# Performance work log

Hardware: AMD Instinct MI355X
Metric: run time of the kernel (lower is better)

Reference implementation:

```python
import jax, jax.numpy as jnp
import numpy as np

N, E, DIN, DH, H, B = 50000, 800000, 128, 32, 8, 512
NEG_SLOPE = 0.2


def glorot(key, shape):
    fan_in, fan_out = shape[0], shape[-1]
    lim = (6.0 / (fan_in + fan_out)) ** 0.5
    return jax.random.uniform(key, shape, jnp.float32, -lim, lim)


def setup_inputs() -> dict:
    key = jax.random.key(0)
    ks = jax.random.split(key, 16)
    x = jax.random.normal(ks[0], (N, DIN), jnp.float32)
    edge_index = jax.random.randint(ks[1], (2, E), 0, N, jnp.int64)
    batch = jnp.sort(jax.random.randint(ks[2], (N,), 0, B, jnp.int64))
    edge_weight = jax.random.uniform(ks[3], (E, 1), jnp.float32)
    # layer 1: GATv2Conv(DIN -> DH, heads=H, edge_dim=1)
    Wl1 = glorot(ks[4], (DIN, H * DH))
    Wr1 = glorot(ks[5], (DIN, H * DH))
    We1 = glorot(ks[6], (1, H * DH))
    att1 = glorot(ks[7], (H, DH))
    b1 = jnp.zeros((H * DH,), jnp.float32)
    # layer 2: GATv2Conv(H*DH -> DH, heads=1, edge_dim=1)
    Wl2 = glorot(ks[8], (H * DH, DH))
    Wr2 = glorot(ks[9], (H * DH, DH))
    We2 = glorot(ks[10], (1, DH))
    att2 = glorot(ks[11], (1, DH))
    b2 = jnp.zeros((DH,), jnp.float32)
    Wfc = glorot(ks[12], (DH, 1))
    bfc = jnp.zeros((1,), jnp.float32)
    return dict(x=x, edge_index=edge_index, batch=batch, edge_weight=edge_weight,
                Wl1=Wl1, Wr1=Wr1, We1=We1, att1=att1, b1=b1,
                Wl2=Wl2, Wr2=Wr2, We2=We2, att2=att2, b2=b2,
                Wfc=Wfc, bfc=bfc)


def gatv2_layer(x, src, dst, ew, Wl, Wr, We, att, bias, heads, out_ch):
    n = x.shape[0]
    xl = (x @ Wl).reshape(n, heads, out_ch)   # source transform
    xr = (x @ Wr).reshape(n, heads, out_ch)   # target transform
    ee = (ew @ We).reshape(-1, heads, out_ch)  # edge attr transform
    z = xl[src] + xr[dst] + ee                 # [E,H,C]
    s = jnp.einsum('ehc,hc->eh', jax.nn.leaky_relu(z, NEG_SLOPE), att)
    # segment softmax over edges sharing the same target node
    m = jax.ops.segment_max(s, dst, num_segments=n)
    ex = jnp.exp(s - m[dst])
    den = jax.ops.segment_sum(ex, dst, num_segments=n)
    alpha = ex / (den[dst] + 1e-16)            # [E,H]
    out = jax.ops.segment_sum(alpha[..., None] * xl[src], dst, num_segments=n)
    return out.reshape(n, heads * out_ch) + bias


def add_self_loops(edge_index, edge_weight, n):
    loops = jnp.arange(n, dtype=edge_index.dtype)
    src = jnp.concatenate([edge_index[0], loops])
    dst = jnp.concatenate([edge_index[1], loops])
    fill = jnp.mean(edge_weight, axis=0, keepdims=True)  # fill_value='mean'
    ew = jnp.concatenate([edge_weight, jnp.broadcast_to(fill, (n, edge_weight.shape[1]))])
    return src, dst, ew


def reference(x, edge_index, batch, edge_weight,
              Wl1, Wr1, We1, att1, b1,
              Wl2, Wr2, We2, att2, b2,
              Wfc, bfc):
    n = x.shape[0]
    src, dst, ew = add_self_loops(edge_index, edge_weight, n)
    h = gatv2_layer(x, src, dst, ew, Wl1, Wr1, We1, att1, b1, H, DH)
    h = jax.nn.relu(h)
    h = gatv2_layer(h, src, dst, ew, Wl2, Wr2, We2, att2, b2, 1, DH)
    feat = jax.nn.relu(h)
    # global mean pool over graphs
    sums = jax.ops.segment_sum(feat, batch, num_segments=B)
    cnt = jax.ops.segment_sum(jnp.ones((n, 1), feat.dtype), batch, num_segments=B)
    feat = sums / jnp.maximum(cnt, 1.0)
    feat = jax.nn.sigmoid(feat)
    return feat @ Wfc + bfc  # [B,1]
```

## Files before the change

### kernel.cpp

```cpp
#include <hip/hip_runtime.h>
#include <math.h>

#define N_NODES 50000
#define N_EDGES 800000
#define D_IN    128
#define D_H     32
#define N_HEADS 8
#define N_GRAPHS 512
#define E_TOT   (N_EDGES + N_NODES)
#define HDIM    (N_HEADS * D_H)
#define NEG_SLOPE 0.2f
#define NSCAN_BLK ((N_NODES + 255) / 256)
#define LOG2E 1.4426950408889634f
#define RESCALE_THR2 11.0f

typedef short bfrag8 __attribute__((ext_vector_type(8)));
typedef float f32x4 __attribute__((ext_vector_type(4)));
typedef float f32x2 __attribute__((ext_vector_type(2)));

#if __has_builtin(__builtin_amdgcn_exp2f)
#define EXP2(x) __builtin_amdgcn_exp2f(x)
#else
#define EXP2(x) exp2f(x)
#endif

__device__ __forceinline__ unsigned short f2b(float x) {
    unsigned u = __float_as_uint(x);
    unsigned r = u + 0x7FFFu + ((u >> 16) & 1u);
    return (unsigned short)(r >> 16);
}
__device__ __forceinline__ f32x2 b2x2(unsigned u) {
    f32x2 v;
    v.x = __uint_as_float(u << 16);
    v.y = __uint_as_float(u & 0xFFFF0000u);
    return v;
}

__device__ __forceinline__ float dpp8_sum(float x) {
    x += __int_as_float(__builtin_amdgcn_mov_dpp(__float_as_int(x), 0xB1, 0xF, 0xF, true));
    x += __int_as_float(__builtin_amdgcn_mov_dpp(__float_as_int(x), 0x4E, 0xF, 0xF, true));
    x += __int_as_float(__builtin_amdgcn_mov_dpp(__float_as_int(x), 0x141, 0xF, 0xF, true));
    return x;
}

#define RS_BLK   512
#define HIST_BLK ((E_TOT + 255) / 256)
#define W1_BLK   (512 * 128 / 256)
#define W2_BLK   (64 * 256 / 256)
__global__ void k_front(const float* __restrict__ ew, const int* __restrict__ ei,
                        const float* __restrict__ Wl1, const float* __restrict__ Wr1,
                        const float* __restrict__ Wl2, const float* __restrict__ Wr2,
                        float* __restrict__ fillsum, int* __restrict__ deg,
                        unsigned short* __restrict__ Wt1,
                        unsigned short* __restrict__ Wt2) {
    __shared__ float ls[4];
    int b = blockIdx.x;
    if (b < RS_BLK) {
        int t = b * 256 + threadIdx.x;
        float s = 0.f;
        for (int i = t; i < N_EDGES; i += RS_BLK * 256) s += ew[i];
        for (int m = 1; m < 64; m <<= 1) s += __shfl_xor(s, m);
        int lane = threadIdx.x & 63, wv = threadIdx.x >> 6;
        if (lane == 0) ls[wv] = s;
        __syncthreads();
        if (threadIdx.x == 0) atomicAdd(fillsum, ls[0] + ls[1] + ls[2] + ls[3]);
    } else if (b < RS_BLK + HIST_BLK) {
        int e = (b - RS_BLK) * 256 + threadIdx.x;
        if (e >= E_TOT) return;
        int dst = (e < N_EDGES) ? ei[N_EDGES + e] : (e - N_EDGES);
        atomicAdd(&deg[dst], 1);
    } else if (b < RS_BLK + HIST_BLK + W1_BLK) {
        int t = (b - RS_BLK - HIST_BLK) * 256 + threadIdx.x;
        int c = t >> 7, k = t & 127;
        float v = (c < 256) ? Wl1[k * 256 + c] : Wr1[k * 256 + (c - 256)];
        Wt1[t] = f2b(v);
    } else {
        int t = (b - RS_BLK - HIST_BLK - W1_BLK) * 256 + threadIdx.x;
        int c = t >> 8, k = t & 255;
        float v = (c < 32) ? Wl2[k * 32 + c] : Wr2[k * 32 + (c - 32)];
        Wt2[t] = f2b(v);
    }
}

__global__ void k_scan1(const int* __restrict__ deg, int* __restrict__ start,
                        int* __restrict__ bsum) {
    __shared__ int sh[256];
    int i = blockIdx.x * 256 + threadIdx.x;
    int v = (i < N_NODES) ? deg[i] : 0;
    sh[threadIdx.x] = v;
    __syncthreads();
    for (int o = 1; o < 256; o <<= 1) {
        int t = (threadIdx.x >= o) ? sh[threadIdx.x - o] : 0;
        __syncthreads();
        sh[threadIdx.x] += t;
        __syncthreads();
    }
    if (i < N_NODES) start[i] = sh[threadIdx.x] - v;
    if (threadIdx.x == 255) bsum[blockIdx.x] = sh[255];
}
__global__ void k_scan2(int* __restrict__ bsum, int nb) {
    __shared__ int sh[256];
    int v = (threadIdx.x < nb) ? bsum[threadIdx.x] : 0;
    sh[threadIdx.x] = v;
    __syncthreads();
    for (int o = 1; o < 256; o <<= 1) {
        int t = (threadIdx.x >= o) ? sh[threadIdx.x - o] : 0;
        __syncthreads();
        sh[threadIdx.x] += t;
        __syncthreads();
    }
    if (threadIdx.x < nb) bsum[threadIdx.x] = sh[threadIdx.x] - v;
}
__global__ void k_scan3(int* __restrict__ start, const int* __restrict__ bsum,
                        int* __restrict__ cur) {
    int i = blockIdx.x * 256 + threadIdx.x;
    if (i < N_NODES) {
        int v = start[i] + bsum[blockIdx.x];
        start[i] = v;
        cur[i] = v;
    }
}

__global__ void k_scatter(const int* __restrict__ ei, const float* __restrict__ ew,
                          const float* __restrict__ fillsum,
                          int* __restrict__ cur, int2* __restrict__ csr) {
    int e = blockIdx.x * blockDim.x + threadIdx.x;
    if (e >= E_TOT) return;
    int src, dst; float w;
    if (e < N_EDGES) { src = ei[e]; dst = ei[N_EDGES + e]; w = ew[e]; }
    else { src = dst = e - N_EDGES; w = fillsum[0] * (1.0f / N_EDGES); }
    int pos = atomicAdd(&cur[dst], 1);
    csr[pos] = make_int2(src, __float_as_int(w));
}

__global__ __launch_bounds__(256) void k_gemm1(
    const float* __restrict__ A, const unsigned short* __restrict__ Bt,
    unsigned short* __restrict__ C, int M)
{
    const int KC = 128, NN = 512;
    __shared__ unsigned short A_lds[128][KC + 8];
    __shared__ unsigned short B_lds[128][KC + 8];
    int row0 = blockIdx.y * 128, col0 = blockIdx.x * 128;
    int tid = threadIdx.x;
    for (int idx = tid; idx < 128 * 32; idx += 256) {
        int r = idx >> 5, c4 = idx & 31;
        int gr = row0 + r;
        float4 v = {0.f, 0.f, 0.f, 0.f};
        if (gr < M) v = ((const float4*)(A + (size_t)gr * KC))[c4];
        ushort4 o;
        o.x = f2b(v.x); o.y = f2b(v.y); o.z = f2b(v.z); o.w = f2b(v.w);
        *(ushort4*)&A_lds[r][c4 * 4] = o;
    }
    for (int idx = tid; idx < 128 * 16; idx += 256) {
        int r = idx >> 4, ch = idx & 15;
        uint4 v = *(const uint4*)(Bt + (size_t)(col0 + r) * KC + ch * 8);
        *(uint4*)&B_lds[r][ch * 8] = v;
    }
    __syncthreads();

    int wid = tid >> 6, lane = tid & 63;
    int wy = wid >> 1, wx = wid & 1;
    int lr = lane & 15, lh = lane >> 4;
    f32x4 acc[4][4] = {};
    #pragma unroll
    for (int k0 = 0; k0 < KC; k0 += 32) {
        bfrag8 af[4], bf[4];
        #pragma unroll
        for (int i = 0; i < 4; ++i) {
            af[i] = *(const bfrag8*)&A_lds[64 * wy + 16 * i + lr][k0 + lh * 8];
            bf[i] = *(const bfrag8*)&B_lds[64 * wx + 16 * i + lr][k0 + lh * 8];
        }
        #pragma unroll
        for (int mi = 0; mi < 4; ++mi)
            #pragma unroll
            for (int ni = 0; ni < 4; ++ni)
                acc[mi][ni] = __builtin_amdgcn_mfma_f32_16x16x32_bf16(af[mi], bf[ni], acc[mi][ni], 0, 0, 0);
    }
    #pragma unroll
    for (int mi = 0; mi < 4; ++mi) {
        #pragma unroll
        for (int ni = 0; ni < 4; ++ni) {
            #pragma unroll
            for (int r = 0; r < 4; ++r) {
                int row = row0 + 64 * wy + 16 * mi + lh * 4 + r;
                if (row < M)
                    C[(size_t)row * NN + col0 + 64 * wx + 16 * ni + lr] = f2b(acc[mi][ni][r]);
            }
        }
    }
}

__global__ __launch_bounds__(256) void k_gemm2(
    const unsigned short* __restrict__ A, const unsigned short* __restrict__ Bt,
    unsigned short* __restrict__ C, int M)
{
    const int KC = 256, NN = 64;
    __shared__ unsigned short A_lds[64][KC + 8];
    __shared__ unsigned short B_lds[64][KC + 8];
    int row0 = blockIdx.y * 64, col0 = 0;
    int tid = threadIdx.x;
    const int CPR = KC / 8;
    for (int idx = tid; idx < 64 * CPR; idx += 256) {
        int r = idx / CPR, ch = idx % CPR;
        int gr = row0 + r;
        uint4 v = {0u, 0u, 0u, 0u};
        if (gr < M) v = *(const uint4*)(A + (size_t)gr * KC + ch * 8);
        *(uint4*)&A_lds[r][ch * 8] = v;
    }
    for (int idx = tid; idx < 64 * CPR; idx += 256) {
        int r = idx / CPR, ch = idx % CPR;
        uint4 v = *(const uint4*)(Bt + (size_t)(col0 + r) * KC + ch * 8);
        *(uint4*)&B_lds[r][ch * 8] = v;
    }
    __syncthreads();

    int wid = tid >> 6, lane = tid & 63;
    int wy = wid >> 1, wx = wid & 1;
    int lr = lane & 15, lh = lane >> 4;
    f32x4 acc[2][2] = {};
    #pragma unroll
    for (int k0 = 0; k0 < KC; k0 += 32) {
        bfrag8 a0 = *(const bfrag8*)&A_lds[32 * wy + lr][k0 + lh * 8];
        bfrag8 a1 = *(const bfrag8*)&A_lds[32 * wy + 16 + lr][k0 + lh * 8];
        bfrag8 b0 = *(const bfrag8*)&B_lds[32 * wx + lr][k0 + lh * 8];
        bfrag8 b1 = *(const bfrag8*)&B_lds[32 * wx + 16 + lr][k0 + lh * 8];
        acc[0][0] = __builtin_amdgcn_mfma_f32_16x16x32_bf16(a0, b0, acc[0][0], 0, 0, 0);
        acc[0][1] = __builtin_amdgcn_mfma_f32_16x16x32_bf16(a0, b1, acc[0][1], 0, 0, 0);
        acc[1][0] = __builtin_amdgcn_mfma_f32_16x16x32_bf16(a1, b0, acc[1][0], 0, 0, 0);
        acc[1][1] = __builtin_amdgcn_mfma_f32_16x16x32_bf16(a1, b1, acc[1][1], 0, 0, 0);
    }
    #pragma unroll
    for (int mt = 0; mt < 2; ++mt) {
        #pragma unroll
        for (int nt = 0; nt < 2; ++nt) {
            #pragma unroll
            for (int r = 0; r < 4; ++r) {
                int row = row0 + 32 * wy + 16 * mt + lh * 4 + r;
                if (row < M)
                    C[(size_t)row * NN + col0 + 32 * wx + 16 * nt + lr] = f2b(acc[mt][nt][r]);
            }
        }
    }
}

__global__ __launch_bounds__(256) void k_gat1(
    const unsigned short* __restrict__ xlr,
    const int* __restrict__ start, const int* __restrict__ deg,
    const int2* __restrict__ csr,
    const float* __restrict__ We, const float* __restrict__ att,
    const float* __restrict__ b1, unsigned short* __restrict__ out1)
{
    int wid = (blockIdx.x * blockDim.x + threadIdx.x) >> 6;
    int lane = threadIdx.x & 63;
    if (wid >= N_NODES) return;
    f32x2 we01 = ((const f32x2*)We)[2 * lane],  we23 = ((const f32x2*)We)[2 * lane + 1];
    f32x2 at01 = ((const f32x2*)att)[2 * lane], at23 = ((const f32x2*)att)[2 * lane + 1];
    at01 *= LOG2E; at23 *= LOG2E;
    uint2 xru = *(const uint2*)(xlr + (size_t)wid * 512 + 256 + 4 * lane);
    f32x2 xr01 = b2x2(xru.x), xr23 = b2x2(xru.y);
    int s0 = start[wid], dg = deg[wid];
    const int2* ep = csr + s0;
    float m = -1e30f, d = 0.f;
    f32x2 acc01 = {0.f, 0.f}, acc23 = {0.f, 0.f};

    int dmax = dg - 1;
    int2 e0 = ep[0];
    int2 e1 = ep[1 < dmax ? 1 : dmax];
    int2 e2 = ep[2 < dmax ? 2 : dmax];
    int2 e3 = ep[3 < dmax ? 3 : dmax];
    uint2 r0 = *(const uint2*)(xlr + ((size_t)e0.x << 9) + 4 * lane);
    uint2 r1 = *(const uint2*)(xlr + ((size_t)e1.x << 9) + 4 * lane);
    uint2 r2 = *(const uint2*)(xlr + ((size_t)e2.x << 9) + 4 * lane);
    uint2 r3 = *(const uint2*)(xlr + ((size_t)e3.x << 9) + 4 * lane);

    for (int j = 0; j < dg; j += 4) {
        float w0 = __int_as_float(e0.y), w1 = __int_as_float(e1.y);
        float w2 = __int_as_float(e2.y), w3 = __int_as_float(e3.y);
        f32x2 a001 = b2x2(r0.x), a023 = b2x2(r0.y);
        f32x2 a101 = b2x2(r1.x), a123 = b2x2(r1.y);
        f32x2 a201 = b2x2(r2.x), a223 = b2x2(r2.y);
        f32x2 a301 = b2x2(r3.x), a323 = b2x2(r3.y);
        int jn = j + 4;
        if (jn < dg) {
            e0 = ep[jn];
            e1 = ep[jn + 1 < dmax ? jn + 1 : dmax];
            e2 = ep[jn + 2 < dmax ? jn + 2 : dmax];
            e3 = ep[jn + 3 < dmax ? jn + 3 : dmax];
            r0 = *(const uint2*)(xlr + ((size_t)e0.x << 9) + 4 * lane);
            r1 = *(const uint2*)(xlr + ((size_t)e1.x << 9) + 4 * lane);
            r2 = *(const uint2*)(xlr + ((size_t)e2.x << 9) + 4 * lane);
            r3 = *(const uint2*)(xlr + ((size_t)e3.x << 9) + 4 * lane);
        }
        f32x2 z, lz, ww, pv;
        ww = (f32x2){w0, w0}; pv = (f32x2){0.f, 0.f};
        z = a001 + __builtin_elementwise_fma(ww, we01, xr01);
        lz = __builtin_elementwise_max(z, z * NEG_SLOPE);
        pv = __builtin_elementwise_fma(lz, at01, pv);
        z = a023 + __builtin_elementwise_fma(ww, we23, xr23);
        lz = __builtin_elementwise_max(z, z * NEG_SLOPE);
        pv = __builtin_elementwise_fma(lz, at23, pv);
        float p0 = pv.x + pv.y;
        ww = (f32x2){w1, w1}; pv = (f32x2){0.f, 0.f};
        z = a101 + __builtin_elementwise_fma(ww, we01, xr01);
        lz = __builtin_elementwise_max(z, z * NEG_SLOPE);
        pv = __builtin_elementwise_fma(lz, at01, pv);
        z = a123 + __builtin_elementwise_fma(ww, we23, xr23);
        lz = __builtin_elementwise_max(z, z * NEG_SLOPE);
        pv = __builtin_elementwise_fma(lz, at23, pv);
        float p1 = pv.x + pv.y;
        ww = (f32x2){w2, w2}; pv = (f32x2){0.f, 0.f};
        z = a201 + __builtin_elementwise_fma(ww, we01, xr01);
        lz = __builtin_elementwise_max(z, z * NEG_SLOPE);
        pv = __builtin_elementwise_fma(lz, at01, pv);
        z = a223 + __builtin_elementwise_fma(ww, we23, xr23);
        lz = __builtin_elementwise_max(z, z * NEG_SLOPE);
        pv = __builtin_elementwise_fma(lz, at23, pv);
        float p2 = pv.x + pv.y;
        ww = (f32x2){w3, w3}; pv = (f32x2){0.f, 0.f};
        z = a301 + __builtin_elementwise_fma(ww, we01, xr01);
        lz = __builtin_elementwise_max(z, z * NEG_SLOPE);
        pv = __builtin_elementwise_fma(lz, at01, pv);
        z = a323 + __builtin_elementwise_fma(ww, we23, xr23);
        lz = __builtin_elementwise_max(z, z * NEG_SLOPE);
        pv = __builtin_elementwise_fma(lz, at23, pv);
        float p3 = pv.x + pv.y;
        p0 = dpp8_sum(p0); p1 = dpp8_sum(p1);
        p2 = dpp8_sum(p2); p3 = dpp8_sum(p3);
        if (j + 1 >= dg) p1 = -1e30f;
        if (j + 2 >= dg) p2 = -1e30f;
        if (j + 3 >= dg) p3 = -1e30f;
        float pm = fmaxf(fmaxf(p0, p1), fmaxf(p2, p3));
        if (__any(pm > m + RESCALE_THR2)) {
            float nm = fmaxf(m, pm);
            float sc = EXP2(m - nm);
            d *= sc;
            acc01 *= sc; acc23 *= sc;
            m = nm;
        }
        float q0 = EXP2(p0 - m), q1 = EXP2(p1 - m);
        float q2 = EXP2(p2 - m), q3 = EXP2(p3 - m);
        d += (q0 + q1) + (q2 + q3);
        f32x2 qq;
        qq = (f32x2){q0, q0};
        acc01 = __builtin_elementwise_fma(qq, a001, acc01);
        acc23 = __builtin_elementwise_fma(qq, a023, acc23);
        qq = (f32x2){q1, q1};
        acc01 = __builtin_elementwise_fma(qq, a101, acc01);
        acc23 = __builtin_elementwise_fma(qq, a123, acc23);
        qq = (f32x2){q2, q2};
        acc01 = __builtin_elementwise_fma(qq, a201, acc01);
        acc23 = __builtin_elementwise_fma(qq, a223, acc23);
        qq = (f32x2){q3, q3};
        acc01 = __builtin_elementwise_fma(qq, a301, acc01);
        acc23 = __builtin_elementwise_fma(qq, a323, acc23);
    }
    float inv = 1.f / (d + 1e-16f);
    f32x2 b01 = ((const f32x2*)b1)[2 * lane], b23 = ((const f32x2*)b1)[2 * lane + 1];
    ushort4 o;
    o.x = f2b(fmaxf(fmaf(acc01.x, inv, b01.x), 0.f));
    o.y = f2b(fmaxf(fmaf(acc01.y, inv, b01.y), 0.f));
    o.z = f2b(fmaxf(fmaf(acc23.x, inv, b23.x), 0.f));
    o.w = f2b(fmaxf(fmaf(acc23.y, inv, b23.y), 0.f));
    *(ushort4*)(out1 + (size_t)wid * 256 + 4 * lane) = o;
}

__global__ __launch_bounds__(256) void k_gat2(
    const unsigned short* __restrict__ xlr2,
    const int* __restrict__ start, const int* __restrict__ deg,
    const int2* __restrict__ csr,
    const float* __restrict__ We, const float* __restrict__ att,
    const float* __restrict__ b2, const int* __restrict__ batch,
    float* __restrict__ pool, float* __restrict__ cnt)
{
    int gt = blockIdx.x * blockDim.x + threadIdx.x;
    int i = gt >> 3, g = gt & 7;
    if (i >= N_NODES) return;
    f32x2 we01 = ((const f32x2*)We)[2 * g],  we23 = ((const f32x2*)We)[2 * g + 1];
    f32x2 at01 = ((const f32x2*)att)[2 * g], at23 = ((const f32x2*)att)[2 * g + 1];
    at01 *= LOG2E; at23 *= LOG2E;
    uint2 xru = *(const uint2*)(xlr2 + (size_t)i * 64 + 32 + 4 * g);
    f32x2 xr01 = b2x2(xru.x), xr23 = b2x2(xru.y);
    int s0 = start[i], dg = deg[i];
    const int2* ep = csr + s0;
    float m = -1e30f, d = 0.f;
    f32x2 acc01 = {0.f, 0.f}, acc23 = {0.f, 0.f};

    int2 ec0 = ep[0];
    int2 ec1 = ep[dg > 1 ? 1 : 0];
    uint2 ra0 = *(const uint2*)(xlr2 + ((size_t)ec0.x << 6) + 4 * g);
    uint2 ra1 = *(const uint2*)(xlr2 + ((size_t)ec1.x << 6) + 4 * g);

    for (int j = 0; j < dg; j += 2) {
        int2 c0 = ec0, c1 = ec1;
        uint2 A0 = ra0, A1 = ra1;
        int jn = j + 2;
        if (jn < dg) {
            ec0 = ep[jn];
            ec1 = ep[(jn + 1 < dg) ? jn + 1 : jn];
            ra0 = *(const uint2*)(xlr2 + ((size_t)ec0.x << 6) + 4 * g);
            ra1 = *(const uint2*)(xlr2 + ((size_t)ec1.x << 6) + 4 * g);
        }
        float w0 = __int_as_float(c0.y), w1 = __int_as_float(c1.y);
        f32x2 ww0 = {w0, w0}, ww1 = {w1, w1};
        f32x2 a001 = b2x2(A0.x), a023 = b2x2(A0.y);
        f32x2 a101 = b2x2(A1.x), a123 = b2x2(A1.y);
        f32x2 p0v = {0.f, 0.f}, p1v = {0.f, 0.f}, z, lz;
        z = a001 + __builtin_elementwise_fma(ww0, we01, xr01);
        lz = __builtin_elementwise_max(z, z * NEG_SLOPE);
        p0v = __builtin_elementwise_fma(lz, at01, p0v);
        z = a023 + __builtin_elementwise_fma(ww0, we23, xr23);
        lz = __builtin_elementwise_max(z, z * NEG_SLOPE);
        p0v = __builtin_elementwise_fma(lz, at23, p0v);
        z = a101 + __builtin_elementwise_fma(ww1, we01, xr01);
        lz = __builtin_elementwise_max(z, z * NEG_SLOPE);
        p1v = __builtin_elementwise_fma(lz, at01, p1v);
        z = a123 + __builtin_elementwise_fma(ww1, we23, xr23);
        lz = __builtin_elementwise_max(z, z * NEG_SLOPE);
        p1v = __builtin_elementwise_fma(lz, at23, p1v);
        float p0 = dpp8_sum(p0v.x + p0v.y);
        float p1 = dpp8_sum(p1v.x + p1v.y);
        if (j + 1 >= dg) p1 = -1e30f;
        float pm = fmaxf(p0, p1);
        if (__any(pm > m + RESCALE_THR2)) {
            float nm = fmaxf(m, pm);
            float sc = EXP2(m - nm);
            d *= sc;
            acc01 *= sc; acc23 *= sc;
            m = nm;
        }
        float q0 = EXP2(p0 - m), q1 = EXP2(p1 - m);
        d += q0 + q1;
        f32x2 qq0 = {q0, q0}, qq1 = {q1, q1};
        acc01 = __builtin_elementwise_fma(qq0, a001, acc01);
        acc23 = __builtin_elementwise_fma(qq0, a023, acc23);
        acc01 = __builtin_elementwise_fma(qq1, a101, acc01);
        acc23 = __builtin_elementwise_fma(qq1, a123, acc23);
    }
    float inv = 1.f / (d + 1e-16f);
    f32x2 b01 = ((const f32x2*)b2)[2 * g], b23 = ((const f32x2*)b2)[2 * g + 1];
    float vx = fmaxf(fmaf(acc01.x, inv, b01.x), 0.f);
    float vy = fmaxf(fmaf(acc01.y, inv, b01.y), 0.f);
    float vz = fmaxf(fmaf(acc23.x, inv, b23.x), 0.f);
    float vw = fmaxf(fmaf(acc23.y, inv, b23.y), 0.f);
    int b = batch[i];
    float* o = pool + (size_t)b * D_H + g * 4;
    atomicAdd(o + 0, vx);
    atomicAdd(o + 1, vy);
    atomicAdd(o + 2, vz);
    atomicAdd(o + 3, vw);
    if (g == 0) atomicAdd(&cnt[b], 1.0f);
}

__global__ void k_final(const float* __restrict__ pool, const float* __restrict__ cnt,
                        const float* __restrict__ Wfc, const float* __restrict__ bfc,
                        float* __restrict__ out)
{
    int b = blockIdx.x * blockDim.x + threadIdx.x;
    if (b >= N_GRAPHS) return;
    float c = cnt[b]; c = c > 1.f ? c : 1.f;
    float acc = 0.f;
    #pragma unroll
    for (int j = 0; j < D_H; ++j) {
        float f = pool[b * D_H + j] / c;
        f = 1.f / (1.f + __expf(-f));
        acc = fmaf(f, Wfc[j], acc);
    }
    out[b] = acc + bfc[0];
}

extern "C" void kernel_launch(void* const* d_in, const int* in_sizes, int n_in,
                              void* d_out, int out_size, void* d_ws, size_t ws_size,
                              hipStream_t stream)
{
    const float* x    = (const float*)d_in[0];
    const int*   ei   = (const int*)  d_in[1];
    const int*   batch= (const int*)  d_in[2];
    const float* ew   = (const float*)d_in[3];
    const float* Wl1  = (const float*)d_in[4];
    const float* Wr1  = (const float*)d_in[5];
    const float* We1  = (const float*)d_in[6];
    const float* att1 = (const float*)d_in[7];
    const float* b1   = (const float*)d_in[8];
    const float* Wl2  = (const float*)d_in[9];
    const float* Wr2  = (const float*)d_in[10];
    const float* We2  = (const float*)d_in[11];
    const float* att2 = (const float*)d_in[12];
    const float* b2   = (const float*)d_in[13];
    const float* Wfc  = (const float*)d_in[14];
    const float* bfc  = (const float*)d_in[15];
    float* out = (float*)d_out;

    float* ws = (float*)d_ws;
    size_t off = 0;
    auto take = [&](size_t n) -> float* {
        float* p = ws + off;
        off = (off + n + 63) & ~(size_t)63;
        return p;
    };
    float* fillsum = take(1);
    int*   deg  = (int*)take(N_NODES);
    float* cnt  = take(N_GRAPHS);
    float* pool = take((size_t)N_GRAPHS * D_H);
    size_t zero_elems = off;
    int*   start = (int*)take(N_NODES);
    int*   cur   = (int*)take(N_NODES);
    int*   bsum  = (int*)take(256);
    int2*  csr   = (int2*)take((size_t)E_TOT * 2);
    unsigned short* Wt1  = (unsigned short*)take(512 * 128 / 2);
    unsigned short* Wt2  = (unsigned short*)take(64 * 256 / 2);
    unsigned short* xlr1 = (unsigned short*)take((size_t)N_NODES * 512 / 2);
    unsigned short* out1 = (unsigned short*)take((size_t)N_NODES * 256 / 2);
    unsigned short* xlr2 = (unsigned short*)take((size_t)N_NODES * 64 / 2);
    (void)ws_size; (void)in_sizes; (void)n_in; (void)out_size;

    hipMemsetAsync(d_ws, 0, zero_elems * sizeof(float), stream);

    k_front<<<RS_BLK + HIST_BLK + W1_BLK + W2_BLK, 256, 0, stream>>>(
        ew, ei, Wl1, Wr1, Wl2, Wr2, fillsum, deg, Wt1, Wt2);

    k_scan1<<<NSCAN_BLK, 256, 0, stream>>>(deg, start, bsum);
    k_scan2<<<1, 256, 0, stream>>>(bsum, NSCAN_BLK);
    k_scan3<<<NSCAN_BLK, 256, 0, stream>>>(start, bsum, cur);
    k_scatter<<<(E_TOT + 255) / 256, 256, 0, stream>>>(ei, ew, fillsum, cur, csr);

    k_gemm1<<<dim3(512 / 128, (N_NODES + 127) / 128), 256, 0, stream>>>(
        x, Wt1, xlr1, N_NODES);

    k_gat1<<<(N_NODES * 64 + 255) / 256, 256, 0, stream>>>(
        xlr1, start, deg, csr, We1, att1, b1, out1);

    k_gemm2<<<dim3(1, (N_NODES + 63) / 64), 256, 0, stream>>>(
        out1, Wt2, xlr2, N_NODES);

    k_gat2<<<((size_t)N_NODES * 8 + 255) / 256, 256, 0, stream>>>(
        xlr2, start, deg, csr, We2, att2, b2, batch, pool, cnt);

    k_final<<<(N_GRAPHS + 255) / 256, 256, 0, stream>>>(pool, cnt, Wfc, bfc, out);
}
```

Baseline: 329.9 us.

## Merge scan kernels into one block and fuse edge scatter with GEMM1

Replaces the three-kernel degree prefix scan with a single 1024-thread block scan. The CSR scatter is fused into the first GEMM launch: blocks are interleaved so two of every three do edge scatter and one does a GEMM tile, letting the atomic-bound scatter overlap with the compute-bound GEMM. The CSR buffer is padded with four zero entries so the GAT kernels' prefetch loads no longer need per-index clamping. This removes several launch boundaries and some index math, at the cost of a serial single-block scan and mixed block roles.

```diff
diff --git a/kernel.cpp b/kernel.cpp
--- a/kernel.cpp
+++ b/kernel.cpp
@@ -10,7 +10,6 @@
 #define E_TOT   (N_EDGES + N_NODES)
 #define HDIM    (N_HEADS * D_H)
 #define NEG_SLOPE 0.2f
-#define NSCAN_BLK ((N_NODES + 255) / 256)
 #define LOG2E 1.4426950408889634f
 #define RESCALE_THR2 11.0f
 
@@ -82,66 +81,74 @@
     }
 }
 
-__global__ void k_scan1(const int* __restrict__ deg, int* __restrict__ start,
-                        int* __restrict__ bsum) {
-    __shared__ int sh[256];
-    int i = blockIdx.x * 256 + threadIdx.x;
-    int v = (i < N_NODES) ? deg[i] : 0;
-    sh[threadIdx.x] = v;
+#define SCAN_CH ((N_NODES + 1023) / 1024)
+__global__ __launch_bounds__(1024) void k_scan_all(
+    const int* __restrict__ deg, int* __restrict__ start,
+    int* __restrict__ cur, int2* __restrict__ csr)
+{
+    __shared__ int part[1024];
+    int t = threadIdx.x;
+    int base = t * SCAN_CH;
+    int s = 0;
+    for (int k = 0; k < SCAN_CH; ++k) {
+        int i = base + k;
+        if (i < N_NODES) s += deg[i];
+    }
+    part[t] = s;
     __syncthreads();
-    for (int o = 1; o < 256; o <<= 1) {
-        int t = (threadIdx.x >= o) ? sh[threadIdx.x - o] : 0;
+    for (int o = 1; o < 1024; o <<= 1) {
+        int v = (t >= o) ? part[t - o] : 0;
         __syncthreads();
-        sh[threadIdx.x] += t;
+        part[t] += v;
         __syncthreads();
     }
-    if (i < N_NODES) start[i] = sh[threadIdx.x] - v;
-    if (threadIdx.x == 255) bsum[blockIdx.x] = sh[255];
-}
-__global__ void k_scan2(int* __restrict__ bsum, int nb) {
-    __shared__ int sh[256];
-    int v = (threadIdx.x < nb) ? bsum[threadIdx.x] : 0;
-    sh[threadIdx.x] = v;
-    __syncthreads();
-    for (int o = 1; o < 256; o <<= 1) {
-        int t = (threadIdx.x >= o) ? sh[threadIdx.x - o] : 0;
-        __syncthreads();
-        sh[threadIdx.x] += t;
-        __syncthreads();
-    }
-    if (threadIdx.x < nb) bsum[threadIdx.x] = sh[threadIdx.x] - v;
-}
-__global__ void k_scan3(int* __restrict__ start, const int* __restrict__ bsum,
-                        int* __restrict__ cur) {
-    int i = blockIdx.x * 256 + threadIdx.x;
-    if (i < N_NODES) {
-        int v = start[i] + bsum[blockIdx.x];
-        start[i] = v;
-        cur[i] = v;
-    }
-}
-
-__global__ void k_scatter(const int* __restrict__ ei, const float* __restrict__ ew,
-                          const float* __restrict__ fillsum,
-                          int* __restrict__ cur, int2* __restrict__ csr) {
-    int e = blockIdx.x * blockDim.x + threadIdx.x;
-    if (e >= E_TOT) return;
-    int src, dst; float w;
-    if (e < N_EDGES) { src = ei[e]; dst = ei[N_EDGES + e]; w = ew[e]; }
-    else { src = dst = e - N_EDGES; w = fillsum[0] * (1.0f / N_EDGES); }
-    int pos = atomicAdd(&cur[dst], 1);
-    csr[pos] = make_int2(src, __float_as_int(w));
-}
-
-__global__ __launch_bounds__(256) void k_gemm1(
+    int run = (t == 0) ? 0 : part[t - 1];
+    for (int k = 0; k < SCAN_CH; ++k) {
+        int i = base + k;
+        if (i < N_NODES) {
+            start[i] = run;
+            cur[i] = run;
+            run += deg[i];
+        }
+    }
+    if (t == 0) {
+        csr[E_TOT]     = make_int2(0, 0);
+        csr[E_TOT + 1] = make_int2(0, 0);
+        csr[E_TOT + 2] = make_int2(0, 0);
+        csr[E_TOT + 3] = make_int2(0, 0);
+    }
+}
+
+#define G1_BLOCKS 1564
+#define SC_BLOCKS ((E_TOT + 255) / 256)
+#define HY_TOT    4985
+__global__ __launch_bounds__(256) void k_gemm1_scatter(
     const float* __restrict__ A, const unsigned short* __restrict__ Bt,
-    unsigned short* __restrict__ C, int M)
-{
-    const int KC = 128, NN = 512;
+    unsigned short* __restrict__ C,
+    const int* __restrict__ ei, const float* __restrict__ ew,
+    const float* __restrict__ fillsum, int* __restrict__ cur,
+    int2* __restrict__ csr)
+{
+    const int KC = 128, NN = 512, M = N_NODES;
     __shared__ unsigned short A_lds[128][KC + 8];
     __shared__ unsigned short B_lds[128][KC + 8];
-    int row0 = blockIdx.y * 128, col0 = blockIdx.x * 128;
+    int bid = blockIdx.x;
     int tid = threadIdx.x;
+    if (bid % 3 != 0) {
+        int sid = bid - bid / 3 - 1;
+        if (sid >= SC_BLOCKS) return;
+        int e = sid * 256 + tid;
+        if (e >= E_TOT) return;
+        int src, dst; float w;
+        if (e < N_EDGES) { src = ei[e]; dst = ei[N_EDGES + e]; w = ew[e]; }
+        else { src = dst = e - N_EDGES; w = fillsum[0] * (1.0f / N_EDGES); }
+        int pos = atomicAdd(&cur[dst], 1);
+        csr[pos] = make_int2(src, __float_as_int(w));
+        return;
+    }
+    int gid = bid / 3;
+    if (gid >= G1_BLOCKS) return;
+    int row0 = (gid >> 2) * 128, col0 = (gid & 3) * 128;
     for (int idx = tid; idx < 128 * 32; idx += 256) {
         int r = idx >> 5, c4 = idx & 31;
         int gr = row0 + r;
@@ -263,11 +270,7 @@
     float m = -1e30f, d = 0.f;
     f32x2 acc01 = {0.f, 0.f}, acc23 = {0.f, 0.f};
 
-    int dmax = dg - 1;
-    int2 e0 = ep[0];
-    int2 e1 = ep[1 < dmax ? 1 : dmax];
-    int2 e2 = ep[2 < dmax ? 2 : dmax];
-    int2 e3 = ep[3 < dmax ? 3 : dmax];
+    int2 e0 = ep[0], e1 = ep[1], e2 = ep[2], e3 = ep[3];
     uint2 r0 = *(const uint2*)(xlr + ((size_t)e0.x << 9) + 4 * lane);
     uint2 r1 = *(const uint2*)(xlr + ((size_t)e1.x << 9) + 4 * lane);
     uint2 r2 = *(const uint2*)(xlr + ((size_t)e2.x << 9) + 4 * lane);
@@ -282,10 +285,7 @@
         f32x2 a301 = b2x2(r3.x), a323 = b2x2(r3.y);
         int jn = j + 4;
         if (jn < dg) {
-            e0 = ep[jn];
-            e1 = ep[jn + 1 < dmax ? jn + 1 : dmax];
-            e2 = ep[jn + 2 < dmax ? jn + 2 : dmax];
-            e3 = ep[jn + 3 < dmax ? jn + 3 : dmax];
+            e0 = ep[jn]; e1 = ep[jn + 1]; e2 = ep[jn + 2]; e3 = ep[jn + 3];
             r0 = *(const uint2*)(xlr + ((size_t)e0.x << 9) + 4 * lane);
             r1 = *(const uint2*)(xlr + ((size_t)e1.x << 9) + 4 * lane);
             r2 = *(const uint2*)(xlr + ((size_t)e2.x << 9) + 4 * lane);
@@ -385,8 +385,7 @@
     float m = -1e30f, d = 0.f;
     f32x2 acc01 = {0.f, 0.f}, acc23 = {0.f, 0.f};
 
-    int2 ec0 = ep[0];
-    int2 ec1 = ep[dg > 1 ? 1 : 0];
+    int2 ec0 = ep[0], ec1 = ep[1];
     uint2 ra0 = *(const uint2*)(xlr2 + ((size_t)ec0.x << 6) + 4 * g);
     uint2 ra1 = *(const uint2*)(xlr2 + ((size_t)ec1.x << 6) + 4 * g);
 
@@ -395,8 +394,7 @@
         uint2 A0 = ra0, A1 = ra1;
         int jn = j + 2;
         if (jn < dg) {
-            ec0 = ep[jn];
-            ec1 = ep[(jn + 1 < dg) ? jn + 1 : jn];
+            ec0 = ep[jn]; ec1 = ep[jn + 1];
             ra0 = *(const uint2*)(xlr2 + ((size_t)ec0.x << 6) + 4 * g);
             ra1 = *(const uint2*)(xlr2 + ((size_t)ec1.x << 6) + 4 * g);
         }
@@ -504,8 +502,7 @@
     size_t zero_elems = off;
     int*   start = (int*)take(N_NODES);
     int*   cur   = (int*)take(N_NODES);
-    int*   bsum  = (int*)take(256);
-    int2*  csr   = (int2*)take((size_t)E_TOT * 2);
+    int2*  csr   = (int2*)take((size_t)(E_TOT + 4) * 2);
     unsigned short* Wt1  = (unsigned short*)take(512 * 128 / 2);
     unsigned short* Wt2  = (unsigned short*)take(64 * 256 / 2);
     unsigned short* xlr1 = (unsigned short*)take((size_t)N_NODES * 512 / 2);
@@ -518,13 +515,10 @@
     k_front<<<RS_BLK + HIST_BLK + W1_BLK + W2_BLK, 256, 0, stream>>>(
         ew, ei, Wl1, Wr1, Wl2, Wr2, fillsum, deg, Wt1, Wt2);
 
-    k_scan1<<<NSCAN_BLK, 256, 0, stream>>>(deg, start, bsum);
-    k_scan2<<<1, 256, 0, stream>>>(bsum, NSCAN_BLK);
-    k_scan3<<<NSCAN_BLK, 256, 0, stream>>>(start, bsum, cur);
-    k_scatter<<<(E_TOT + 255) / 256, 256, 0, stream>>>(ei, ew, fillsum, cur, csr);
-
-    k_gemm1<<<dim3(512 / 128, (N_NODES + 127) / 128), 256, 0, stream>>>(
-        x, Wt1, xlr1, N_NODES);
+    k_scan_all<<<1, 1024, 0, stream>>>(deg, start, cur, csr);
+
+    k_gemm1_scatter<<<HY_TOT, 256, 0, stream>>>(
+        x, Wt1, xlr1, ei, ew, fillsum, cur, csr);
 
     k_gat1<<<(N_NODES * 64 + 255) / 256, 256, 0, stream>>>(
         xlr1, start, deg, csr, We1, att1, b1, out1);
```

Result: slower. 391.6 us (+18.7%).

## Fuse CSR scatter into GEMM1 launch and pad CSR to drop clamped prefetch

Applied to the files above, without the earlier changes.

Merges the edge-scatter kernel and the first GEMM into one launch, interleaving blocks so that one in three runs a GEMM tile and the rest scatter edges. The memory-bound atomic scatter then overlaps with the compute-bound GEMM and one launch is removed. The CSR array also gets four zeroed padding entries, so the GAT kernels' prefetch can read past a node's degree without index clamping. The over-read entries point at node 0 and are discarded; the block-index arithmetic adds a few instructions per block.

```diff
diff --git a/kernel.cpp b/kernel.cpp
--- a/kernel.cpp
+++ b/kernel.cpp
@@ -112,36 +112,51 @@
     if (threadIdx.x < nb) bsum[threadIdx.x] = sh[threadIdx.x] - v;
 }
 __global__ void k_scan3(int* __restrict__ start, const int* __restrict__ bsum,
-                        int* __restrict__ cur) {
+                        int* __restrict__ cur, int2* __restrict__ csr) {
     int i = blockIdx.x * 256 + threadIdx.x;
     if (i < N_NODES) {
         int v = start[i] + bsum[blockIdx.x];
         start[i] = v;
         cur[i] = v;
     }
-}
-
-__global__ void k_scatter(const int* __restrict__ ei, const float* __restrict__ ew,
-                          const float* __restrict__ fillsum,
-                          int* __restrict__ cur, int2* __restrict__ csr) {
-    int e = blockIdx.x * blockDim.x + threadIdx.x;
-    if (e >= E_TOT) return;
-    int src, dst; float w;
-    if (e < N_EDGES) { src = ei[e]; dst = ei[N_EDGES + e]; w = ew[e]; }
-    else { src = dst = e - N_EDGES; w = fillsum[0] * (1.0f / N_EDGES); }
-    int pos = atomicAdd(&cur[dst], 1);
-    csr[pos] = make_int2(src, __float_as_int(w));
-}
-
-__global__ __launch_bounds__(256) void k_gemm1(
+    if (i == 0) {
+        csr[E_TOT]     = make_int2(0, 0);
+        csr[E_TOT + 1] = make_int2(0, 0);
+        csr[E_TOT + 2] = make_int2(0, 0);
+        csr[E_TOT + 3] = make_int2(0, 0);
+    }
+}
+
+#define G1_BLOCKS 1564
+#define SC_BLOCKS ((E_TOT + 255) / 256)
+#define HY_TOT    4985
+__global__ __launch_bounds__(256) void k_gemm1_scatter(
     const float* __restrict__ A, const unsigned short* __restrict__ Bt,
-    unsigned short* __restrict__ C, int M)
+    unsigned short* __restrict__ C,
+    const int* __restrict__ ei, const float* __restrict__ ew,
+    const float* __restrict__ fillsum, int* __restrict__ cur,
+    int2* __restrict__ csr)
 {
-    const int KC = 128, NN = 512;
+    const int KC = 128, NN = 512, M = N_NODES;
     __shared__ unsigned short A_lds[128][KC + 8];
     __shared__ unsigned short B_lds[128][KC + 8];
-    int row0 = blockIdx.y * 128, col0 = blockIdx.x * 128;
+    int bid = blockIdx.x;
     int tid = threadIdx.x;
+    if (bid % 3 != 0) {
+        int sid = bid - bid / 3 - 1;
+        if (sid >= SC_BLOCKS) return;
+        int e = sid * 256 + tid;
+        if (e >= E_TOT) return;
+        int src, dst; float w;
+        if (e < N_EDGES) { src = ei[e]; dst = ei[N_EDGES + e]; w = ew[e]; }
+        else { src = dst = e - N_EDGES; w = fillsum[0] * (1.0f / N_EDGES); }
+        int pos = atomicAdd(&cur[dst], 1);
+        csr[pos] = make_int2(src, __float_as_int(w));
+        return;
+    }
+    int gid = bid / 3;
+    if (gid >= G1_BLOCKS) return;
+    int row0 = (gid >> 2) * 128, col0 = (gid & 3) * 128;
     for (int idx = tid; idx < 128 * 32; idx += 256) {
         int r = idx >> 5, c4 = idx & 31;
         int gr = row0 + r;
@@ -263,11 +278,7 @@
     float m = -1e30f, d = 0.f;
     f32x2 acc01 = {0.f, 0.f}, acc23 = {0.f, 0.f};
 
-    int dmax = dg - 1;
-    int2 e0 = ep[0];
-    int2 e1 = ep[1 < dmax ? 1 : dmax];
-    int2 e2 = ep[2 < dmax ? 2 : dmax];
-    int2 e3 = ep[3 < dmax ? 3 : dmax];
+    int2 e0 = ep[0], e1 = ep[1], e2 = ep[2], e3 = ep[3];
     uint2 r0 = *(const uint2*)(xlr + ((size_t)e0.x << 9) + 4 * lane);
     uint2 r1 = *(const uint2*)(xlr + ((size_t)e1.x << 9) + 4 * lane);
     uint2 r2 = *(const uint2*)(xlr + ((size_t)e2.x << 9) + 4 * lane);
@@ -282,10 +293,7 @@
         f32x2 a301 = b2x2(r3.x), a323 = b2x2(r3.y);
         int jn = j + 4;
         if (jn < dg) {
-            e0 = ep[jn];
-            e1 = ep[jn + 1 < dmax ? jn + 1 : dmax];
-            e2 = ep[jn + 2 < dmax ? jn + 2 : dmax];
-            e3 = ep[jn + 3 < dmax ? jn + 3 : dmax];
+            e0 = ep[jn]; e1 = ep[jn + 1]; e2 = ep[jn + 2]; e3 = ep[jn + 3];
             r0 = *(const uint2*)(xlr + ((size_t)e0.x << 9) + 4 * lane);
             r1 = *(const uint2*)(xlr + ((size_t)e1.x << 9) + 4 * lane);
             r2 = *(const uint2*)(xlr + ((size_t)e2.x << 9) + 4 * lane);
@@ -385,8 +393,7 @@
     float m = -1e30f, d = 0.f;
     f32x2 acc01 = {0.f, 0.f}, acc23 = {0.f, 0.f};
 
-    int2 ec0 = ep[0];
-    int2 ec1 = ep[dg > 1 ? 1 : 0];
+    int2 ec0 = ep[0], ec1 = ep[1];
     uint2 ra0 = *(const uint2*)(xlr2 + ((size_t)ec0.x << 6) + 4 * g);
     uint2 ra1 = *(const uint2*)(xlr2 + ((size_t)ec1.x << 6) + 4 * g);
 
@@ -395,8 +402,7 @@
         uint2 A0 = ra0, A1 = ra1;
         int jn = j + 2;
         if (jn < dg) {
-            ec0 = ep[jn];
-            ec1 = ep[(jn + 1 < dg) ? jn + 1 : jn];
+            ec0 = ep[jn]; ec1 = ep[jn + 1];
             ra0 = *(const uint2*)(xlr2 + ((size_t)ec0.x << 6) + 4 * g);
             ra1 = *(const uint2*)(xlr2 + ((size_t)ec1.x << 6) + 4 * g);
         }
@@ -505,7 +511,7 @@
     int*   start = (int*)take(N_NODES);
     int*   cur   = (int*)take(N_NODES);
     int*   bsum  = (int*)take(256);
-    int2*  csr   = (int2*)take((size_t)E_TOT * 2);
+    int2*  csr   = (int2*)take((size_t)(E_TOT + 4) * 2);
     unsigned short* Wt1  = (unsigned short*)take(512 * 128 / 2);
     unsigned short* Wt2  = (unsigned short*)take(64 * 256 / 2);
     unsigned short* xlr1 = (unsigned short*)take((size_t)N_NODES * 512 / 2);
@@ -520,11 +526,10 @@
 
     k_scan1<<<NSCAN_BLK, 256, 0, stream>>>(deg, start, bsum);
     k_scan2<<<1, 256, 0, stream>>>(bsum, NSCAN_BLK);
-    k_scan3<<<NSCAN_BLK, 256, 0, stream>>>(start, bsum, cur);
-    k_scatter<<<(E_TOT + 255) / 256, 256, 0, stream>>>(ei, ew, fillsum, cur, csr);
-
-    k_gemm1<<<dim3(512 / 128, (N_NODES + 127) / 128), 256, 0, stream>>>(
-        x, Wt1, xlr1, N_NODES);
+    k_scan3<<<NSCAN_BLK, 256, 0, stream>>>(start, bsum, cur, csr);
+
+    k_gemm1_scatter<<<HY_TOT, 256, 0, stream>>>(
+        x, Wt1, xlr1, ei, ew, fillsum, cur, csr);
 
     k_gat1<<<(N_NODES * 64 + 255) / 256, 256, 0, stream>>>(
         xlr1, start, deg, csr, We1, att1, b1, out1);
```

Result: faster. 277.4 us (-15.9%).
